# Kernel tuning notes

Measured on AMD Instinct MI355X. Metric: run time of the kernel, lower is better.

The kernel has to match this reference:

```python
import jax, jax.numpy as jnp
import numpy as np

B, T, D, H = 2, 2048, 2048, 16
DK = D // H  # 128
THETA = 10000.0


def _rope_angles():
    inv_freq = 1.0 / (THETA ** (np.arange(0, DK, 2, dtype=np.float32) / DK))  # (DK/2,)
    pos = np.arange(T, dtype=np.float32)
    freqs = pos[:, None] * inv_freq[None, :]  # (T, DK/2)
    return jnp.asarray(np.broadcast_to(freqs[None], (B, T, DK // 2)).copy())


def setup_inputs() -> dict:
    key = jax.random.key(0)
    k1, k2, k3 = jax.random.split(key, 3)
    x = jax.random.normal(k1, (B, T, D), dtype=jnp.float32)
    Wqkv = jax.random.normal(k2, (D, 3 * D), dtype=jnp.float32) * (D ** -0.5)
    Wout = jax.random.normal(k3, (D, D), dtype=jnp.float32) * (D ** -0.5)
    return {"x": x, "freqs": _rope_angles(), "Wqkv": Wqkv, "Wout": Wout}


def _apply_rope(xh, cos, sin):
    # xh: (B,T,H,DK); consecutive pairs form complex numbers (torch view_as_complex)
    xr = xh[..., 0::2]  # (B,T,H,DK/2) real parts
    xi = xh[..., 1::2]  # imag parts
    # cos/sin: (B,T,1,DK/2)
    or_ = xr * cos - xi * sin
    oi_ = xr * sin + xi * cos
    return jnp.stack([or_, oi_], axis=-1).reshape(xh.shape)


def reference(x, freqs, Wqkv, Wout):
    qkv = x @ Wqkv  # (B,T,3D)
    qkv = qkv.reshape(B, T, H, 3 * DK)
    q, k, v = qkv[..., :DK], qkv[..., DK:2 * DK], qkv[..., 2 * DK:]
    cos = jnp.cos(freqs)[:, :, None, :]
    sin = jnp.sin(freqs)[:, :, None, :]
    q = _apply_rope(q, cos, sin)
    k = _apply_rope(k, cos, sin)
    # (B,H,T,DK)
    q = q.transpose(0, 2, 1, 3)
    k = k.transpose(0, 2, 1, 3)
    v = v.transpose(0, 2, 1, 3)
    scores = jnp.einsum('bhqd,bhkd->bhqk', q, k) * (DK ** -0.5)
    causal = jnp.tril(jnp.ones((T, T), dtype=bool))
    scores = jnp.where(causal[None, None], scores, -jnp.inf)
    attn = jax.nn.softmax(scores, axis=-1)
    attn = jnp.nan_to_num(attn)
    out = jnp.einsum('bhqk,bhkd->bhqd', attn, v)  # (B,H,T,DK)
    out = out.transpose(0, 2, 1, 3).reshape(B, T, D)
    return out @ Wout
```

## Files before the change

kernel.cpp:

```cpp
#include <hip/hip_runtime.h>
#include <cstdint>

#define BATCH   2
#define T_SEQ   2048
#define NH      16
#define DK      128
#define DMODEL  2048
#define NQKV    6144

using short8 = __attribute__((ext_vector_type(8))) short;
using f32x4  = __attribute__((ext_vector_type(4))) float;

__device__ __forceinline__ float bf2f(unsigned short u) {
    union { float f; uint32_t i; } x; x.i = ((uint32_t)u) << 16; return x.f;
}
__device__ __forceinline__ unsigned short f2bf(float f) {
    union { float f; uint32_t i; } x; x.f = f;
    uint32_t r = x.i + 0x7fffu + ((x.i >> 16) & 1u);
    return (unsigned short)(r >> 16);
}

__device__ __forceinline__ void async_load16(const unsigned short* g, unsigned short* l) {
    __builtin_amdgcn_global_load_lds(
        (const __attribute__((address_space(1))) unsigned int*)g,
        (__attribute__((address_space(3))) unsigned int*)l,
        16, 0, 0);
}


__global__ void cast_x_kernel(const float* __restrict__ x,
                              unsigned short* __restrict__ xb, int n4) {
    int i = blockIdx.x * 256 + threadIdx.x;
    if (i >= n4) return;
    float4 v = ((const float4*)x)[i];
    ushort4 o;
    o.x = f2bf(v.x); o.y = f2bf(v.y); o.z = f2bf(v.z); o.w = f2bf(v.w);
    ((ushort4*)xb)[i] = o;
}

__global__ void wtrans_kernel(const float* __restrict__ W,
                              unsigned short* __restrict__ WT, int K, int N) {
    __shared__ unsigned short tile[64][65];
    int k0 = blockIdx.y * 64, n0 = blockIdx.x * 64;
    for (int it = 0; it < 16; ++it) {
        int idx = it * 256 + threadIdx.x;
        int r = idx >> 6, c = idx & 63;
        tile[r][c] = f2bf(W[(size_t)(k0 + r) * N + n0 + c]);
    }
    __syncthreads();
    for (int it = 0; it < 16; ++it) {
        int idx = it * 256 + threadIdx.x;
        int r = idx >> 6, c = idx & 63;
        WT[(size_t)(n0 + r) * K + k0 + c] = tile[c][r];
    }
}

template <int MODE>
__global__ __launch_bounds__(256) void gemm_bt_kernel(
    const unsigned short* __restrict__ A, const unsigned short* __restrict__ BT,
    float* __restrict__ Cout,
    unsigned short* __restrict__ qraw, unsigned short* __restrict__ kraw,
    unsigned short* __restrict__ vtb,
    int M, int N, int K) {
    __shared__ __align__(16) unsigned short As[128 * 64];
    __shared__ __align__(16) unsigned short Bs[128 * 64];
    const int tid = threadIdx.x;
    const int w = tid >> 6, lane = tid & 63;
    const int lrow = lane & 15, quad = lane >> 4;
    const int m0 = blockIdx.y * 128, n0 = blockIdx.x * 128;
    const int wm = (w & 1) * 64, wn = (w >> 1) * 64;

    f32x4 acc[4][4];
#pragma unroll
    for (int a = 0; a < 4; ++a)
#pragma unroll
        for (int b = 0; b < 4; ++b) acc[a][b] = (f32x4){0.f, 0.f, 0.f, 0.f};

    for (int k0 = 0; k0 < K; k0 += 64) {
#pragma unroll
        for (int j = 0; j < 4; ++j) {
            int c   = (w * 4 + j) * 64 + lane;
            int row = c >> 3;
            int kcg = (c & 7) ^ (row & 7);
            async_load16(A  + (size_t)(m0 + row) * K + k0 + kcg * 8,
                         As + (size_t)(w * 4 + j) * 64 * 8);
            async_load16(BT + (size_t)(n0 + row) * K + k0 + kcg * 8,
                         Bs + (size_t)(w * 4 + j) * 64 * 8);
        }
        __syncthreads();
#pragma unroll
        for (int kk = 0; kk < 2; ++kk) {
            short8 af[4], bfr[4];
#pragma unroll
            for (int mt = 0; mt < 4; ++mt) {
                int row = wm + mt * 16 + lrow;
                int kcs = (kk * 4 + quad) ^ (row & 7);
                af[mt] = *(const short8*)(As + row * 64 + kcs * 8);
            }
#pragma unroll
            for (int nt = 0; nt < 4; ++nt) {
                int row = wn + nt * 16 + lrow;
                int kcs = (kk * 4 + quad) ^ (row & 7);
                bfr[nt] = *(const short8*)(Bs + row * 64 + kcs * 8);
            }
#pragma unroll
            for (int mt = 0; mt < 4; ++mt)
#pragma unroll
                for (int nt = 0; nt < 4; ++nt)
                    acc[mt][nt] = __builtin_amdgcn_mfma_f32_16x16x32_bf16(
                        af[mt], bfr[nt], acc[mt][nt], 0, 0, 0);
        }
        __syncthreads();
    }

    if (MODE == 0) {
#pragma unroll
        for (int mt = 0; mt < 4; ++mt)
#pragma unroll
            for (int nt = 0; nt < 4; ++nt)
#pragma unroll
                for (int r = 0; r < 4; ++r) {
                    int row = m0 + wm + mt * 16 + quad * 4 + r;
                    int col = n0 + wn + nt * 16 + lrow;
                    Cout[(size_t)row * N + col] = acc[mt][nt][r];
                }
    } else {
#pragma unroll
        for (int mt = 0; mt < 4; ++mt) {
            int trow = m0 + wm + mt * 16 + quad * 4;
            int bi = trow >> 11;
            int tb = trow & (T_SEQ - 1);
#pragma unroll
            for (int nt = 0; nt < 4; ++nt) {
                int colb = n0 + wn + nt * 16;
                int h    = colb / 384;
                int r3   = colb - h * 384;
                int sec  = r3 >> 7;
                int dk   = (r3 & 127) + lrow;
                if (sec == 0) {
                    unsigned short* dst =
                        qraw + ((size_t)(bi * NH + h) * T_SEQ + tb) * DK + dk;
#pragma unroll
                    for (int r = 0; r < 4; ++r) dst[(size_t)r * DK] = f2bf(acc[mt][nt][r]);
                } else if (sec == 1) {
                    unsigned short* dst =
                        kraw + ((size_t)(bi * NH + h) * T_SEQ + tb) * DK + dk;
#pragma unroll
                    for (int r = 0; r < 4; ++r) dst[(size_t)r * DK] = f2bf(acc[mt][nt][r]);
                } else {
                    ushort4 p;
                    p.x = f2bf(acc[mt][nt][0]); p.y = f2bf(acc[mt][nt][1]);
                    p.z = f2bf(acc[mt][nt][2]); p.w = f2bf(acc[mt][nt][3]);
                    *(ushort4*)(vtb + ((size_t)(bi * NH + h) * DK + dk) * T_SEQ + tb) = p;
                }
            }
        }
    }
}

__global__ void rope_kernel(unsigned short* __restrict__ qraw,
                            unsigned short* __restrict__ kraw,
                            const float* __restrict__ freqs) {
    int linear = blockIdx.x * 256 + threadIdx.x;
    int i  = linear & 63;
    int t  = (linear >> 6) & (T_SEQ - 1);
    int bh = linear >> 17;
    int b  = bh >> 4;
    float f  = freqs[((size_t)b * T_SEQ + t) * 64 + i];
    float cs = __cosf(f), sn = __sinf(f);
    size_t off = ((size_t)bh * T_SEQ + t) * DK + 2 * i;
    ushort2 qp = *(ushort2*)(qraw + off);
    ushort2 kp = *(ushort2*)(kraw + off);
    float qr = bf2f(qp.x), qi = bf2f(qp.y);
    float kr = bf2f(kp.x), ki = bf2f(kp.y);
    ushort2 qo, ko;
    qo.x = f2bf(qr * cs - qi * sn); qo.y = f2bf(qr * sn + qi * cs);
    ko.x = f2bf(kr * cs - ki * sn); ko.y = f2bf(kr * sn + ki * cs);
    *(ushort2*)(qraw + off) = qo;
    *(ushort2*)(kraw + off) = ko;
}

__global__ __launch_bounds__(256) void attn_kernel(
    const unsigned short* __restrict__ qb, const unsigned short* __restrict__ kb,
    const unsigned short* __restrict__ vt, unsigned short* __restrict__ ctx) {
    __shared__ __align__(16) unsigned short Ks[2][64 * 128];
    __shared__ __align__(16) unsigned short Vs[2][128 * 64];
    __shared__ __align__(16) unsigned short pbuf[4][16 * 68];
    const int qt   = 31 - blockIdx.y;
    const int u    = blockIdx.x;
    const int bh   = ((u & 7) << 2) | (u >> 3);
    const int q0   = qt * 64;
    const int w    = threadIdx.x >> 6, lane = threadIdx.x & 63;
    const int lrow = lane & 15, quad = lane >> 4;
    const int qrow = q0 + w * 16;
    const float sc2 = 0.08838834764831845f * 1.4426950408889634f;
    const short8 vone = {16256, 16256, 16256, 16256, 16256, 16256, 16256, 16256};

    short8 aq[4];
    const unsigned short* qbase = qb + ((size_t)bh * T_SEQ + qrow + lrow) * DK;
#pragma unroll
    for (int kk = 0; kk < 4; ++kk)
        aq[kk] = *(const short8*)(qbase + kk * 32 + quad * 8);

    f32x4 o[8];
#pragma unroll
    for (int d = 0; d < 8; ++d) o[d] = (f32x4){0.f, 0.f, 0.f, 0.f};
    f32x4 ol = (f32x4){0.f, 0.f, 0.f, 0.f};

    const unsigned short* kg0 = kb + (size_t)bh * T_SEQ * DK;
    const unsigned short* vg0 = vt + (size_t)bh * DK * T_SEQ;

    auto stage = [&](int kt, int sbuf) {
        const unsigned short* kg = kg0 + (size_t)kt * 64 * DK;
        const unsigned short* vg = vg0 + kt * 64;
        unsigned short* Kd = &Ks[sbuf][0];
        unsigned short* Vd = &Vs[sbuf][0];
#pragma unroll
        for (int j = 0; j < 4; ++j) {
            int c = (w * 4 + j) * 64 + lane;
            int kr_ = c >> 4, kc = (c & 15) ^ (kr_ & 7);
            async_load16(kg + (size_t)kr_ * DK + kc * 8, Kd + c * 8);
            int vr = c >> 3, vc = (c & 7) ^ (vr & 7);
            async_load16(vg + (size_t)vr * T_SEQ + vc * 8, Vd + c * 8);
        }
    };

    stage(0, 0);
    for (int kt = 0; kt <= qt; ++kt) {
        __syncthreads();
        if (kt < qt) stage(kt + 1, (kt + 1) & 1);
        const unsigned short* Kb = &Ks[kt & 1][0];
        const unsigned short* Vb = &Vs[kt & 1][0];

        f32x4 s[4];
#pragma unroll
        for (int nt = 0; nt < 4; ++nt) s[nt] = (f32x4){0.f, 0.f, 0.f, 0.f};
#pragma unroll
        for (int kk = 0; kk < 4; ++kk)
#pragma unroll
            for (int nt = 0; nt < 4; ++nt) {
                int row = nt * 16 + lrow;
                int kc = (kk * 4 + quad) ^ (row & 7);
                short8 bk = *(const short8*)(Kb + row * 128 + kc * 8);
                s[nt] = __builtin_amdgcn_mfma_f32_16x16x32_bf16(aq[kk], bk, s[nt], 0, 0, 0);
            }

        const bool diag = (kt == qt);
        unsigned short* pb = &pbuf[w][0];
#pragma unroll
        for (int nt = 0; nt < 4; ++nt)
#pragma unroll
            for (int r = 0; r < 4; ++r) {
                float p = exp2f(fmaf(s[nt][r], sc2, -12.0f));
                if (diag && (nt * 16 + lrow > w * 16 + quad * 4 + r)) p = 0.f;
                pb[(quad * 4 + r) * 68 + nt * 16 + lrow] = f2bf(p);
            }
        __builtin_amdgcn_s_waitcnt(0xc07f);
        short8 ap[2];
#pragma unroll
        for (int kk2 = 0; kk2 < 2; ++kk2)
            ap[kk2] = *(const short8*)(pb + lrow * 68 + kk2 * 32 + quad * 8);

#pragma unroll
        for (int kk2 = 0; kk2 < 2; ++kk2)
            ol = __builtin_amdgcn_mfma_f32_16x16x32_bf16(ap[kk2], vone, ol, 0, 0, 0);
#pragma unroll
        for (int d = 0; d < 8; ++d)
#pragma unroll
            for (int kk2 = 0; kk2 < 2; ++kk2) {
                int row = d * 16 + lrow;
                int vc = (kk2 * 4 + quad) ^ (row & 7);
                short8 bv = *(const short8*)(Vb + row * 64 + vc * 8);
                o[d] = __builtin_amdgcn_mfma_f32_16x16x32_bf16(ap[kk2], bv, o[d], 0, 0, 0);
            }
    }

    const int b = bh >> 4, h = bh & 15;
    float rl[4];
#pragma unroll
    for (int r = 0; r < 4; ++r) rl[r] = 1.0f / ol[r];
#pragma unroll
    for (int d = 0; d < 8; ++d)
#pragma unroll
        for (int r = 0; r < 4; ++r) {
            int row = qrow + quad * 4 + r;
            ctx[((size_t)(b * T_SEQ + row)) * DMODEL + h * DK + d * 16 + lrow] =
                f2bf(o[d][r] * rl[r]);
        }
}

extern "C" void kernel_launch(void* const* d_in, const int* in_sizes, int n_in,
                              void* d_out, int out_size, void* d_ws, size_t ws_size,
                              hipStream_t stream) {
    const float* x     = (const float*)d_in[0];
    const float* freqs = (const float*)d_in[1];
    const float* Wqkv  = (const float*)d_in[2];
    const float* Wout  = (const float*)d_in[3];
    float* out = (float*)d_out;
    char* ws = (char*)d_ws;
    unsigned short* xb    = (unsigned short*)(ws);
    unsigned short* ctx   = (unsigned short*)(ws);
    unsigned short* wqkvT = (unsigned short*)(ws + 16777216);
    unsigned short* woutT = (unsigned short*)(ws + 41943040);
    unsigned short* qraw  = (unsigned short*)(ws + 50331648);
    unsigned short* kraw  = (unsigned short*)(ws + 67108864);
    unsigned short* vtb   = (unsigned short*)(ws + 83886080);

    cast_x_kernel<<<8192, 256, 0, stream>>>(x, xb, 2097152);
    wtrans_kernel<<<dim3(96, 32), 256, 0, stream>>>(Wqkv, wqkvT, DMODEL, NQKV);
    wtrans_kernel<<<dim3(32, 32), 256, 0, stream>>>(Wout, woutT, DMODEL, DMODEL);
    gemm_bt_kernel<1><<<dim3(48, 32), 256, 0, stream>>>(
        xb, wqkvT, nullptr, qraw, kraw, vtb, BATCH * T_SEQ, NQKV, DMODEL);
    rope_kernel<<<16384, 256, 0, stream>>>(qraw, kraw, freqs);
    attn_kernel<<<dim3(32, 32), 256, 0, stream>>>(qraw, kraw, vtb, ctx);
    gemm_bt_kernel<0><<<dim3(16, 32), 256, 0, stream>>>(
        ctx, woutT, out, nullptr, nullptr, nullptr, BATCH * T_SEQ, DMODEL, DMODEL);
}
```

Measured before the change: 385.0 us.

## Fuse RoPE into QKV GEMM epilogue and merge prep kernels into one launch

Applies the rotary embedding inside the QKV GEMM epilogue: adjacent lanes swap values with a lane shuffle and compute sin/cos in registers, so the separate rope kernel is removed. That kernel read and rewrote all of q and k in global memory. The x cast and both weight transpose/cast kernels are merged into one prep kernel launch, with the job chosen by block index, which cuts launch overhead. The epilogue now does an extra freqs load and a sincos per element, and the even/odd pair must sit in adjacent lanes.

```diff
diff --git a/kernel.cpp b/kernel.cpp
--- a/kernel.cpp
+++ b/kernel.cpp
@@ -27,21 +27,29 @@
         16, 0, 0);
 }
 
-
-__global__ void cast_x_kernel(const float* __restrict__ x,
-                              unsigned short* __restrict__ xb, int n4) {
-    int i = blockIdx.x * 256 + threadIdx.x;
-    if (i >= n4) return;
-    float4 v = ((const float4*)x)[i];
-    ushort4 o;
-    o.x = f2bf(v.x); o.y = f2bf(v.y); o.z = f2bf(v.z); o.w = f2bf(v.w);
-    ((ushort4*)xb)[i] = o;
-}
-
-__global__ void wtrans_kernel(const float* __restrict__ W,
-                              unsigned short* __restrict__ WT, int K, int N) {
+__global__ __launch_bounds__(256) void prep_kernel(
+    const float* __restrict__ x,    unsigned short* __restrict__ xb,
+    const float* __restrict__ Wqkv, unsigned short* __restrict__ wqkvT,
+    const float* __restrict__ Wout, unsigned short* __restrict__ woutT) {
     __shared__ unsigned short tile[64][65];
-    int k0 = blockIdx.y * 64, n0 = blockIdx.x * 64;
+    const int bid = blockIdx.x;
+    if (bid < 8192) {
+        int i = bid * 256 + threadIdx.x;
+        float4 v = ((const float4*)x)[i];
+        ushort4 o;
+        o.x = f2bf(v.x); o.y = f2bf(v.y); o.z = f2bf(v.z); o.w = f2bf(v.w);
+        ((ushort4*)xb)[i] = o;
+        return;
+    }
+    const float* W; unsigned short* WT; int N, n0, k0;
+    const int K = DMODEL;
+    if (bid < 11264) {
+        int b = bid - 8192;  W = Wqkv; WT = wqkvT; N = NQKV;
+        n0 = (b % 96) * 64; k0 = (b / 96) * 64;
+    } else {
+        int b = bid - 11264; W = Wout; WT = woutT; N = DMODEL;
+        n0 = (b & 31) * 64; k0 = (b >> 5) * 64;
+    }
     for (int it = 0; it < 16; ++it) {
         int idx = it * 256 + threadIdx.x;
         int r = idx >> 6, c = idx & 63;
@@ -60,7 +68,7 @@
     const unsigned short* __restrict__ A, const unsigned short* __restrict__ BT,
     float* __restrict__ Cout,
     unsigned short* __restrict__ qraw, unsigned short* __restrict__ kraw,
-    unsigned short* __restrict__ vtb,
+    unsigned short* __restrict__ vtb, const float* __restrict__ freqs,
     int M, int N, int K) {
     __shared__ __align__(16) unsigned short As[128 * 64];
     __shared__ __align__(16) unsigned short Bs[128 * 64];
@@ -137,16 +145,23 @@
                 int r3   = colb - h * 384;
                 int sec  = r3 >> 7;
                 int dk   = (r3 & 127) + lrow;
-                if (sec == 0) {
-                    unsigned short* dst =
-                        qraw + ((size_t)(bi * NH + h) * T_SEQ + tb) * DK + dk;
-#pragma unroll
-                    for (int r = 0; r < 4; ++r) dst[(size_t)r * DK] = f2bf(acc[mt][nt][r]);
-                } else if (sec == 1) {
-                    unsigned short* dst =
-                        kraw + ((size_t)(bi * NH + h) * T_SEQ + tb) * DK + dk;
-#pragma unroll
-                    for (int r = 0; r < 4; ++r) dst[(size_t)r * DK] = f2bf(acc[mt][nt][r]);
+                if (sec < 2) {
+                    unsigned short* dst = (sec == 0 ? qraw : kraw) +
+                        ((size_t)(bi * NH + h) * T_SEQ + tb) * DK + dk;
+                    const int   i    = dk >> 1;
+                    const bool  odd  = dk & 1;
+                    const float* fb  = freqs + ((size_t)bi * T_SEQ + tb) * 64 + i;
+#pragma unroll
+                    for (int r = 0; r < 4; ++r) {
+                        float f = fb[(size_t)r * 64];
+                        float sn, cs;
+                        __sincosf(f, &sn, &cs);
+                        float own = acc[mt][nt][r];
+                        float oth = __shfl_xor(own, 1, 64);
+                        float v = odd ? (oth * sn + own * cs)
+                                      : (own * cs - oth * sn);
+                        dst[(size_t)r * DK] = f2bf(v);
+                    }
                 } else {
                     ushort4 p;
                     p.x = f2bf(acc[mt][nt][0]); p.y = f2bf(acc[mt][nt][1]);
@@ -156,28 +171,6 @@
             }
         }
     }
-}
-
-__global__ void rope_kernel(unsigned short* __restrict__ qraw,
-                            unsigned short* __restrict__ kraw,
-                            const float* __restrict__ freqs) {
-    int linear = blockIdx.x * 256 + threadIdx.x;
-    int i  = linear & 63;
-    int t  = (linear >> 6) & (T_SEQ - 1);
-    int bh = linear >> 17;
-    int b  = bh >> 4;
-    float f  = freqs[((size_t)b * T_SEQ + t) * 64 + i];
-    float cs = __cosf(f), sn = __sinf(f);
-    size_t off = ((size_t)bh * T_SEQ + t) * DK + 2 * i;
-    ushort2 qp = *(ushort2*)(qraw + off);
-    ushort2 kp = *(ushort2*)(kraw + off);
-    float qr = bf2f(qp.x), qi = bf2f(qp.y);
-    float kr = bf2f(kp.x), ki = bf2f(kp.y);
-    ushort2 qo, ko;
-    qo.x = f2bf(qr * cs - qi * sn); qo.y = f2bf(qr * sn + qi * cs);
-    ko.x = f2bf(kr * cs - ki * sn); ko.y = f2bf(kr * sn + ki * cs);
-    *(ushort2*)(qraw + off) = qo;
-    *(ushort2*)(kraw + off) = ko;
 }
 
 __global__ __launch_bounds__(256) void attn_kernel(
@@ -306,13 +299,11 @@
     unsigned short* kraw  = (unsigned short*)(ws + 67108864);
     unsigned short* vtb   = (unsigned short*)(ws + 83886080);
 
-    cast_x_kernel<<<8192, 256, 0, stream>>>(x, xb, 2097152);
-    wtrans_kernel<<<dim3(96, 32), 256, 0, stream>>>(Wqkv, wqkvT, DMODEL, NQKV);
-    wtrans_kernel<<<dim3(32, 32), 256, 0, stream>>>(Wout, woutT, DMODEL, DMODEL);
+    prep_kernel<<<12288, 256, 0, stream>>>(x, xb, Wqkv, wqkvT, Wout, woutT);
     gemm_bt_kernel<1><<<dim3(48, 32), 256, 0, stream>>>(
-        xb, wqkvT, nullptr, qraw, kraw, vtb, BATCH * T_SEQ, NQKV, DMODEL);
-    rope_kernel<<<16384, 256, 0, stream>>>(qraw, kraw, freqs);
+        xb, wqkvT, nullptr, qraw, kraw, vtb, freqs, BATCH * T_SEQ, NQKV, DMODEL);
     attn_kernel<<<dim3(32, 32), 256, 0, stream>>>(qraw, kraw, vtb, ctx);
     gemm_bt_kernel<0><<<dim3(16, 32), 256, 0, stream>>>(
-        ctx, woutT, out, nullptr, nullptr, nullptr, BATCH * T_SEQ, DMODEL, DMODEL);
-}
+        ctx, woutT, out, nullptr, nullptr, nullptr, nullptr,
+        BATCH * T_SEQ, DMODEL, DMODEL);
+}
```

New measurement: 388.6 us. Within noise of the previous version (+0.9%).
